# Optimization experiments

Measured on AMD Instinct MI355X. Metric: run time of the kernel, lower is better.

Reference implementation:

```python
import jax, jax.numpy as jnp
import numpy as np

V, D, H, T, S = 50000, 256, 512, 16, 8192
H2 = H // 2
START, END = 0, 1
NEG = -10000.0


def setup_inputs() -> dict:
    key = jax.random.key(0)
    ks = jax.random.split(key, 16)

    def rn(k, shape, scale=0.1):
        return jax.random.normal(k, shape, dtype=jnp.float32) * scale

    sentence = jax.random.randint(ks[0], (S,), 0, V)
    emb = rn(ks[1], (V, D), 1.0)
    w_ih_f = rn(ks[2], (4 * H2, D)); w_hh_f = rn(ks[3], (4 * H2, H2))
    b_f = rn(ks[4], (4 * H2,))  # b_ih + b_hh fused
    w_ih_b = rn(ks[5], (4 * H2, D)); w_hh_b = rn(ks[6], (4 * H2, H2))
    b_b = rn(ks[7], (4 * H2,))
    h0_f = rn(ks[8], (H2,), 1.0); c0_f = rn(ks[9], (H2,), 1.0)
    h0_b = rn(ks[10], (H2,), 1.0); c0_b = rn(ks[11], (H2,), 1.0)
    w_out = rn(ks[12], (T, H)); b_out = rn(ks[13], (T,))
    trans = jax.random.normal(ks[14], (T, T), dtype=jnp.float32)
    # transition[START, :] = -10000 ; transition[:, END] = -10000
    trans = trans.at[START, :].set(NEG).at[:, END].set(NEG)
    return {"sentence": sentence, "emb": emb,
            "w_ih_f": w_ih_f, "w_hh_f": w_hh_f, "b_f": b_f,
            "w_ih_b": w_ih_b, "w_hh_b": w_hh_b, "b_b": b_b,
            "h0_f": h0_f, "c0_f": c0_f, "h0_b": h0_b, "c0_b": c0_b,
            "w_out": w_out, "b_out": b_out, "trans": trans}


def _lstm(pre, w_hh, h0, c0):
    # pre: [S, 4*H2] precomputed input projections (x @ W_ih^T + b)
    def step(carry, pre_t):
        h, c = carry
        g = pre_t + w_hh @ h
        i, f, gg, o = jnp.split(g, 4)  # torch gate order: i, f, g, o
        i = jax.nn.sigmoid(i); f = jax.nn.sigmoid(f)
        gg = jnp.tanh(gg); o = jax.nn.sigmoid(o)
        c = f * c + i * gg
        h = o * jnp.tanh(c)
        return (h, c), h
    _, hs = jax.lax.scan(step, (h0, c0), pre)
    return hs  # [S, H2]


def reference(sentence, emb, w_ih_f, w_hh_f, b_f, w_ih_b, w_hh_b, b_b,
              h0_f, c0_f, h0_b, c0_b, w_out, b_out, trans):
    x = emb[sentence]                               # [S, D]
    pre_f = x @ w_ih_f.T + b_f                      # [S, 4*H2]
    pre_b = x[::-1] @ w_ih_b.T + b_b                # reverse direction
    hs_f = _lstm(pre_f, w_hh_f, h0_f, c0_f)         # [S, H2]
    hs_b = _lstm(pre_b, w_hh_b, h0_b, c0_b)[::-1]   # [S, H2]
    feats = jnp.concatenate([hs_f, hs_b], axis=-1) @ w_out.T + b_out  # [S, T]

    # Viterbi (max-plus DP), vectorized over the tag dimension.
    init = jnp.full((T,), NEG, dtype=feats.dtype).at[START].set(0.0)

    def vit_step(score, emit_t):
        cand = score[None, :] + trans               # [T_next, T_prev]
        best = jnp.argmax(cand, axis=1)             # backpointers [T]
        score = jnp.max(cand, axis=1) + emit_t
        return score, best

    last, back = jax.lax.scan(vit_step, init, feats)  # back: [S, T] int
    final = last + trans[END]                       # [T]
    best_last = jnp.argmax(final)
    path_score = final[best_last]

    # Backtrack: path[S-1] = best_last, path[t-1] = back[t][path[t]]
    def back_step(tag, bp_t):
        return bp_t[tag], tag
    _, path = jax.lax.scan(back_step, best_last, back, reverse=True)
    return path_score, path
```

## Files before the change

### kernel.cpp

```cpp
#include <hip/hip_runtime.h>
#include <math.h>

#define SLEN 8192
#define DIM  256
#define H2N  256
#define G4   1024
#define NTAG 16
#define NEGV (-10000.0f)

#define OFF_PRE_F   0
#define OFF_PRE_B   (SLEN*G4)
#define OFF_HS_F    (2*SLEN*G4)
#define OFF_HS_B    (2*SLEN*G4 + SLEN*H2N)
#define OFF_FEATS   (2*SLEN*G4 + 2*SLEN*H2N)
#define OFF_MBOX    (OFF_FEATS + SLEN*NTAG)
#define WS_NEEDED   ((size_t)(OFF_MBOX + 1024) * 4)

__global__ __launch_bounds__(256) void gemm_pre(
    const int* __restrict__ sent, const float* __restrict__ emb,
    const float* __restrict__ wf, const float* __restrict__ bf,
    const float* __restrict__ wb, const float* __restrict__ bb,
    float* __restrict__ pre_f, float* __restrict__ pre_b)
{
    const int dir = blockIdx.z;
    const float* w    = dir ? wb : wf;
    const float* bias = dir ? bb : bf;
    float* out        = dir ? pre_b : pre_f;
    const int m0 = blockIdx.x * 64, n0 = blockIdx.y * 64;

    __shared__ float As[16][68];
    __shared__ float Bs[16][68];
    __shared__ int   sidx[64];

    const int tid = threadIdx.x;
    const int tx = tid & 15, ty = tid >> 4;

    if (tid < 64) {
        int m = m0 + tid;
        int pos = dir ? (SLEN - 1 - m) : m;
        sidx[tid] = sent[pos];
    }
    __syncthreads();

    float acc[4][4];
#pragma unroll
    for (int i = 0; i < 4; i++)
#pragma unroll
        for (int j = 0; j < 4; j++) acc[i][j] = 0.f;

    const int lr = tid >> 2, lc = (tid & 3) * 4;

    for (int k0 = 0; k0 < DIM; k0 += 16) {
        float4 av = *(const float4*)(emb + (size_t)sidx[lr] * DIM + k0 + lc);
        float4 bv = *(const float4*)(w + (size_t)(n0 + lr) * DIM + k0 + lc);
        As[lc+0][lr] = av.x; As[lc+1][lr] = av.y; As[lc+2][lr] = av.z; As[lc+3][lr] = av.w;
        Bs[lc+0][lr] = bv.x; Bs[lc+1][lr] = bv.y; Bs[lc+2][lr] = bv.z; Bs[lc+3][lr] = bv.w;
        __syncthreads();
#pragma unroll
        for (int k = 0; k < 16; k++) {
            float4 a4 = *(const float4*)&As[k][ty * 4];
            float4 b4 = *(const float4*)&Bs[k][tx * 4];
            float a[4] = {a4.x, a4.y, a4.z, a4.w};
            float b[4] = {b4.x, b4.y, b4.z, b4.w};
#pragma unroll
            for (int i = 0; i < 4; i++)
#pragma unroll
                for (int j = 0; j < 4; j++) acc[i][j] += a[i] * b[j];
        }
        __syncthreads();
    }

    float4 b4 = *(const float4*)(bias + n0 + tx*4);
#pragma unroll
    for (int i = 0; i < 4; i++) {
        float4 v;
        v.x = acc[i][0] + b4.x; v.y = acc[i][1] + b4.y;
        v.z = acc[i][2] + b4.z; v.w = acc[i][3] + b4.w;
        *(float4*)(out + (size_t)(m0 + ty*4 + i) * G4 + n0 + tx*4) = v;
    }
}

__device__ __forceinline__ float fast_sigmoid(float x) {
    return 1.f / (1.f + __expf(-x));
}
__device__ __forceinline__ float fast_tanh(float x) {
    float xc = fminf(fmaxf(x, -15.f), 15.f);
    float e = __expf(2.f * xc);
    return (e - 1.f) / (e + 1.f);
}

__global__ __launch_bounds__(64) void lstm_kernel(
    const float* __restrict__ pre_f, const float* __restrict__ pre_b,
    const float* __restrict__ whh_f, const float* __restrict__ whh_b,
    const float* __restrict__ h0_f, const float* __restrict__ c0_f,
    const float* __restrict__ h0_b, const float* __restrict__ c0_b,
    float* __restrict__ hs_f, float* __restrict__ hs_b,
    unsigned* __restrict__ mbox)
{
    const int blk = blockIdx.x;
    const int d = blk >> 5, cb = blk & 31;
    const int cell0 = cb * 8;
    const float* pre = d ? pre_b : pre_f;
    const float* whh = d ? whh_b : whh_f;
    const float* h0  = d ? h0_b : h0_f;
    const float* c0  = d ? c0_b : c0_f;
    float* hs        = d ? hs_b : hs_f;

    const int l = threadIdx.x;
    const int r = l >> 1;
    const int half = l & 1;
    const int g = r >> 3, cl = r & 7;
    const int grow = g * 256 + cell0 + cl;

    __shared__ __align__(16) float4 w_pack4[32 * 64];
    __shared__ __align__(16) float  h_lds[256];

    {
        const float4* src = (const float4*)(whh + (size_t)grow * H2N + half * 128);
#pragma unroll
        for (int j = 0; j < 32; j++) w_pack4[j * 64 + l] = src[j];
    }
    ((float4*)h_lds)[l] = ((const float4*)h0)[l];
    float c = (l < 8) ? c0[cell0 + l] : 0.f;
    __syncthreads();

    const float* pre_base = pre + grow;
    float pre_cur = (half == 0) ? pre_base[0] : 0.f;
    const int ai = l & 7;
    unsigned* mb_dir = mbox + d * 512;

    for (int t = 0; t < SLEN; t++) {
        float pre_next = (half == 0 && t < SLEN - 1) ? pre_base[(size_t)(t + 1) * G4] : 0.f;
        const unsigned etag = (((unsigned)t >> 1) & 1u) ^ 1u;
        unsigned* mb = mb_dir + (t & 1) * 256;

        float a0 = pre_cur, a1 = 0.f, a2 = 0.f, a3 = 0.f;
        const float4* hrow4 = (const float4*)(h_lds + half * 128);
#pragma unroll
        for (int j = 0; j < 32; j++) {
            float4 wv = w_pack4[j * 64 + l];
            float4 hv = hrow4[j];
            a0 += wv.x * hv.x; a1 += wv.y * hv.y;
            a2 += wv.z * hv.z; a3 += wv.w * hv.w;
        }
        float sum = (a0 + a1) + (a2 + a3);
        sum += __shfl_xor(sum, 1, 64);

        float s_i = __shfl(sum, 2 * ai, 64);
        float s_f = __shfl(sum, 16 + 2 * ai, 64);
        float s_g = __shfl(sum, 32 + 2 * ai, 64);
        float s_o = __shfl(sum, 48 + 2 * ai, 64);

        if (l < 8) {
            float i_ = fast_sigmoid(s_i);
            float f_ = fast_sigmoid(s_f);
            float g_ = fast_tanh(s_g);
            float o_ = fast_sigmoid(s_o);
            c = f_ * c + i_ * g_;
            float h = o_ * fast_tanh(c);
            unsigned hm = (__float_as_uint(h) & ~1u) | etag;
            __hip_atomic_store(mb + cell0 + l, hm,
                               __ATOMIC_RELAXED, __HIP_MEMORY_SCOPE_AGENT);
            __builtin_nontemporal_store(hm, (unsigned*)hs + (size_t)t * H2N + cell0 + l);
        }

        const unsigned* msrc = mb + 4 * l;
        unsigned v0, v1, v2, v3;
        int spin = 0;
        do {
            v0 = __hip_atomic_load(msrc + 0, __ATOMIC_RELAXED, __HIP_MEMORY_SCOPE_AGENT);
            v1 = __hip_atomic_load(msrc + 1, __ATOMIC_RELAXED, __HIP_MEMORY_SCOPE_AGENT);
            v2 = __hip_atomic_load(msrc + 2, __ATOMIC_RELAXED, __HIP_MEMORY_SCOPE_AGENT);
            v3 = __hip_atomic_load(msrc + 3, __ATOMIC_RELAXED, __HIP_MEMORY_SCOPE_AGENT);
        } while ((((v0 ^ etag) | (v1 ^ etag) | (v2 ^ etag) | (v3 ^ etag)) & 1u)
                 && ++spin < 2000000);

        float4 hv4;
        hv4.x = __uint_as_float(v0); hv4.y = __uint_as_float(v1);
        hv4.z = __uint_as_float(v2); hv4.w = __uint_as_float(v3);
        *(float4*)(h_lds + 4 * l) = hv4;
        __syncthreads();
        pre_cur = pre_next;
    }
}

__global__ __launch_bounds__(256) void feats_kernel(
    const float* __restrict__ hs_f, const float* __restrict__ hs_b,
    const float* __restrict__ w_out, const float* __restrict__ b_out,
    float* __restrict__ feats)
{
    const int rs0 = blockIdx.x * 16;
    const int tid = threadIdx.x;
    const int r = tid >> 4, cc = tid & 15;

    __shared__ float Hs[16][516];
    for (int i = tid; i < 16 * 256; i += 256) {
        int rr = i >> 8, k = i & 255;
        Hs[rr][k]       = hs_f[(size_t)(rs0 + rr) * H2N + k];
        Hs[rr][256 + k] = hs_b[(size_t)(SLEN - 1 - (rs0 + rr)) * H2N + k];
    }
    __syncthreads();

    float acc = 0.f;
    const float* wr = w_out + (size_t)cc * 512;
    const float* hrow = Hs[r];
#pragma unroll 4
    for (int kq = 0; kq < 128; kq++) {
        float4 hv = *(const float4*)(hrow + 4 * kq);
        float4 wv = *(const float4*)(wr + 4 * kq);
        acc += hv.x * wv.x; acc += hv.y * wv.y;
        acc += hv.z * wv.z; acc += hv.w * wv.w;
    }
    feats[(size_t)(rs0 + r) * NTAG + cc] = acc + b_out[cc];
}

__global__ __launch_bounds__(64) void viterbi_kernel(
    const float* __restrict__ feats, const float* __restrict__ trans,
    float* __restrict__ out)
{
    __shared__ unsigned char back_s[SLEN * 8];

    const int lane = threadIdx.x;
    const int nx = lane >> 2, pc = lane & 3;

    float tr[4];
#pragma unroll
    for (int j = 0; j < 4; j++) tr[j] = trans[nx * NTAG + pc * 4 + j];

    float sc = (nx == 0) ? 0.f : NEGV;
    float fe = feats[nx];

    for (int t = 0; t < SLEN; t++) {
        float fe_next = (t < SLEN - 1) ? feats[(size_t)(t + 1) * NTAG + nx] : 0.f;

        float bv; int bi;
#pragma unroll
        for (int j = 0; j < 4; j++) {
            float s = __shfl(sc, 4 * (pc * 4 + j), 64);
            float cand = s + tr[j];
            if (j == 0) { bv = cand; bi = pc * 4; }
            else if (cand > bv) { bv = cand; bi = pc * 4 + j; }
        }
#pragma unroll
        for (int off = 1; off < 4; off <<= 1) {
            float ov = __shfl_xor(bv, off, 64);
            int   oi = __shfl_xor(bi, off, 64);
            if (ov > bv || (ov == bv && oi < bi)) { bv = ov; bi = oi; }
        }
        int bi_part = __shfl(bi, (nx | 1) * 4, 64);
        if (pc == 0 && (nx & 1) == 0)
            back_s[t * 8 + (nx >> 1)] = (unsigned char)((bi & 15) | (bi_part << 4));
        sc = bv + fe;
        fe = fe_next;
    }

    float bestv = 0.f; int besti = 0;
#pragma unroll
    for (int j = 0; j < NTAG; j++) {
        float sj = __shfl(sc, 4 * j, 64);
        float fj = sj + trans[1 * NTAG + j];
        if (j == 0) { bestv = fj; besti = 0; }
        else if (fj > bestv) { bestv = fj; besti = j; }
    }
    __syncthreads();

    if (lane == 0) {
        out[0] = bestv;
        int cur = besti;
        for (int t = SLEN - 1; t >= 1; t--) {
            out[1 + t] = (float)cur;
            unsigned char byte = back_s[t * 8 + (cur >> 1)];
            cur = (cur & 1) ? (byte >> 4) : (byte & 15);
        }
        out[1] = (float)cur;
    }
}

extern "C" void kernel_launch(void* const* d_in, const int* in_sizes, int n_in,
                              void* d_out, int out_size, void* d_ws, size_t ws_size,
                              hipStream_t stream) {
    const int*   sent   = (const int*)d_in[0];
    const float* emb    = (const float*)d_in[1];
    const float* w_ih_f = (const float*)d_in[2];
    const float* w_hh_f = (const float*)d_in[3];
    const float* b_f    = (const float*)d_in[4];
    const float* w_ih_b = (const float*)d_in[5];
    const float* w_hh_b = (const float*)d_in[6];
    const float* b_b    = (const float*)d_in[7];
    const float* h0_f   = (const float*)d_in[8];
    const float* c0_f   = (const float*)d_in[9];
    const float* h0_b   = (const float*)d_in[10];
    const float* c0_b   = (const float*)d_in[11];
    const float* w_out  = (const float*)d_in[12];
    const float* b_out  = (const float*)d_in[13];
    const float* trans  = (const float*)d_in[14];
    float* out = (float*)d_out;

    if (ws_size < WS_NEEDED) return;

    float* ws = (float*)d_ws;
    float* pre_f = ws + OFF_PRE_F;
    float* pre_b = ws + OFF_PRE_B;
    float* hs_f  = ws + OFF_HS_F;
    float* hs_b  = ws + OFF_HS_B;
    float* feats = ws + OFF_FEATS;
    unsigned* mbox = (unsigned*)(ws + OFF_MBOX);

    gemm_pre<<<dim3(128, 16, 2), 256, 0, stream>>>(sent, emb, w_ih_f, b_f, w_ih_b, b_b, pre_f, pre_b);
    lstm_kernel<<<64, 64, 0, stream>>>(pre_f, pre_b, w_hh_f, w_hh_b,
                                       h0_f, c0_f, h0_b, c0_b, hs_f, hs_b, mbox);
    feats_kernel<<<512, 256, 0, stream>>>(hs_f, hs_b, w_out, b_out, feats);
    viterbi_kernel<<<1, 64, 0, stream>>>(feats, trans, out);
}
```

Before: 21.19 ms.

## Interleave forward and backward LSTM directions in one block to hide exchange latency

Each block now processes both LSTM directions for its 8 cells, with the grid halved from 64 to 32 blocks. The cross-block mailbox poll for one direction is issued right after its publish and checked only after the other direction's matvec, so the global-memory round trip overlaps useful work. __syncthreads is replaced by an s_waitcnt lgkmcnt fence, which is enough because each block is a single 64-lane wavefront. The cost is double the LDS use per block and serial per-block work for two directions, which lengthens each step if the mailbox latency was not the bottleneck.

```diff
diff --git a/kernel.cpp b/kernel.cpp
--- a/kernel.cpp
+++ b/kernel.cpp
@@ -88,6 +88,12 @@
     float e = __expf(2.f * xc);
     return (e - 1.f) / (e + 1.f);
 }
+__device__ __forceinline__ unsigned aload(const unsigned* p) {
+    return __hip_atomic_load(p, __ATOMIC_RELAXED, __HIP_MEMORY_SCOPE_AGENT);
+}
+__device__ __forceinline__ void lds_fence() {
+    asm volatile("s_waitcnt lgkmcnt(0)" ::: "memory");
+}
 
 __global__ __launch_bounds__(64) void lstm_kernel(
     const float* __restrict__ pre_f, const float* __restrict__ pre_b,
@@ -97,14 +103,8 @@
     float* __restrict__ hs_f, float* __restrict__ hs_b,
     unsigned* __restrict__ mbox)
 {
-    const int blk = blockIdx.x;
-    const int d = blk >> 5, cb = blk & 31;
+    const int cb = blockIdx.x;
     const int cell0 = cb * 8;
-    const float* pre = d ? pre_b : pre_f;
-    const float* whh = d ? whh_b : whh_f;
-    const float* h0  = d ? h0_b : h0_f;
-    const float* c0  = d ? c0_b : c0_f;
-    float* hs        = d ? hs_b : hs_f;
 
     const int l = threadIdx.x;
     const int r = l >> 1;
@@ -112,75 +112,142 @@
     const int g = r >> 3, cl = r & 7;
     const int grow = g * 256 + cell0 + cl;
 
-    __shared__ __align__(16) float4 w_pack4[32 * 64];
-    __shared__ __align__(16) float  h_lds[256];
+    __shared__ __align__(16) float4 wf4[32 * 64];
+    __shared__ __align__(16) float4 wb4[32 * 64];
+    __shared__ __align__(16) float  hf_lds[256];
+    __shared__ __align__(16) float  hb_lds[256];
 
     {
-        const float4* src = (const float4*)(whh + (size_t)grow * H2N + half * 128);
-#pragma unroll
-        for (int j = 0; j < 32; j++) w_pack4[j * 64 + l] = src[j];
-    }
-    ((float4*)h_lds)[l] = ((const float4*)h0)[l];
-    float c = (l < 8) ? c0[cell0 + l] : 0.f;
+        const float4* sf = (const float4*)(whh_f + (size_t)grow * H2N + half * 128);
+        const float4* sb = (const float4*)(whh_b + (size_t)grow * H2N + half * 128);
+#pragma unroll
+        for (int j = 0; j < 32; j++) { wf4[j * 64 + l] = sf[j]; wb4[j * 64 + l] = sb[j]; }
+    }
+    ((float4*)hf_lds)[l] = ((const float4*)h0_f)[l];
+    ((float4*)hb_lds)[l] = ((const float4*)h0_b)[l];
+    float c_f = (l < 8) ? c0_f[cell0 + l] : 0.f;
+    float c_b = (l < 8) ? c0_b[cell0 + l] : 0.f;
     __syncthreads();
 
-    const float* pre_base = pre + grow;
-    float pre_cur = (half == 0) ? pre_base[0] : 0.f;
+    const float* pf_base = pre_f + grow;
+    const float* pb_base = pre_b + grow;
+    float pf_cur = (half == 0) ? pf_base[0] : 0.f;
+    float pb_cur = (half == 0) ? pb_base[0] : 0.f;
     const int ai = l & 7;
-    unsigned* mb_dir = mbox + d * 512;
-
-    for (int t = 0; t < SLEN; t++) {
-        float pre_next = (half == 0 && t < SLEN - 1) ? pre_base[(size_t)(t + 1) * G4] : 0.f;
-        const unsigned etag = (((unsigned)t >> 1) & 1u) ^ 1u;
-        unsigned* mb = mb_dir + (t & 1) * 256;
-
-        float a0 = pre_cur, a1 = 0.f, a2 = 0.f, a3 = 0.f;
-        const float4* hrow4 = (const float4*)(h_lds + half * 128);
-#pragma unroll
-        for (int j = 0; j < 32; j++) {
-            float4 wv = w_pack4[j * 64 + l];
-            float4 hv = hrow4[j];
-            a0 += wv.x * hv.x; a1 += wv.y * hv.y;
-            a2 += wv.z * hv.z; a3 += wv.w * hv.w;
-        }
-        float sum = (a0 + a1) + (a2 + a3);
-        sum += __shfl_xor(sum, 1, 64);
-
-        float s_i = __shfl(sum, 2 * ai, 64);
-        float s_f = __shfl(sum, 16 + 2 * ai, 64);
-        float s_g = __shfl(sum, 32 + 2 * ai, 64);
-        float s_o = __shfl(sum, 48 + 2 * ai, 64);
-
-        if (l < 8) {
-            float i_ = fast_sigmoid(s_i);
-            float f_ = fast_sigmoid(s_f);
-            float g_ = fast_tanh(s_g);
-            float o_ = fast_sigmoid(s_o);
-            c = f_ * c + i_ * g_;
-            float h = o_ * fast_tanh(c);
-            unsigned hm = (__float_as_uint(h) & ~1u) | etag;
-            __hip_atomic_store(mb + cell0 + l, hm,
-                               __ATOMIC_RELAXED, __HIP_MEMORY_SCOPE_AGENT);
-            __builtin_nontemporal_store(hm, (unsigned*)hs + (size_t)t * H2N + cell0 + l);
-        }
-
-        const unsigned* msrc = mb + 4 * l;
-        unsigned v0, v1, v2, v3;
-        int spin = 0;
-        do {
-            v0 = __hip_atomic_load(msrc + 0, __ATOMIC_RELAXED, __HIP_MEMORY_SCOPE_AGENT);
-            v1 = __hip_atomic_load(msrc + 1, __ATOMIC_RELAXED, __HIP_MEMORY_SCOPE_AGENT);
-            v2 = __hip_atomic_load(msrc + 2, __ATOMIC_RELAXED, __HIP_MEMORY_SCOPE_AGENT);
-            v3 = __hip_atomic_load(msrc + 3, __ATOMIC_RELAXED, __HIP_MEMORY_SCOPE_AGENT);
-        } while ((((v0 ^ etag) | (v1 ^ etag) | (v2 ^ etag) | (v3 ^ etag)) & 1u)
-                 && ++spin < 2000000);
-
-        float4 hv4;
-        hv4.x = __uint_as_float(v0); hv4.y = __uint_as_float(v1);
-        hv4.z = __uint_as_float(v2); hv4.w = __uint_as_float(v3);
-        *(float4*)(h_lds + 4 * l) = hv4;
-        __syncthreads();
-        pre_cur = pre_next;
+    unsigned* mbf = mbox;
+    unsigned* mbb = mbox + 512;
+
+    uint4 vf = {0, 0, 0, 0}, vb = {0, 0, 0, 0};
+
+    for (int i = 0; i < SLEN; i++) {
+        const unsigned etag = (((unsigned)i >> 1) & 1u) ^ 1u;
+        unsigned* mbf_cur = mbf + (i & 1) * 256;
+        unsigned* mbb_cur = mbb + (i & 1) * 256;
+
+        if (i > 0) {
+            const unsigned ptag = (((unsigned)(i - 1) >> 1) & 1u) ^ 1u;
+            const unsigned* src = mbb + ((i - 1) & 1) * 256 + 4 * l;
+            int spin = 0;
+            while ((((vb.x ^ ptag) | (vb.y ^ ptag) | (vb.z ^ ptag) | (vb.w ^ ptag)) & 1u)
+                   && ++spin < 2000000) {
+                vb.x = aload(src + 0); vb.y = aload(src + 1);
+                vb.z = aload(src + 2); vb.w = aload(src + 3);
+            }
+            float4 hv; hv.x = __uint_as_float(vb.x); hv.y = __uint_as_float(vb.y);
+            hv.z = __uint_as_float(vb.z); hv.w = __uint_as_float(vb.w);
+            *(float4*)(hb_lds + 4 * l) = hv;
+            lds_fence();
+        }
+
+        float pb_next = (half == 0 && i < SLEN - 1) ? pb_base[(size_t)(i + 1) * G4] : 0.f;
+        {
+            float a0 = pb_cur, a1 = 0.f, a2 = 0.f, a3 = 0.f;
+            const float4* hrow4 = (const float4*)(hb_lds + half * 128);
+#pragma unroll
+            for (int j = 0; j < 32; j++) {
+                float4 wv = wb4[j * 64 + l];
+                float4 hv = hrow4[j];
+                a0 += wv.x * hv.x; a1 += wv.y * hv.y;
+                a2 += wv.z * hv.z; a3 += wv.w * hv.w;
+            }
+            float sum = (a0 + a1) + (a2 + a3);
+            sum += __shfl_xor(sum, 1, 64);
+            float s_i = __shfl(sum, 2 * ai, 64);
+            float s_f = __shfl(sum, 16 + 2 * ai, 64);
+            float s_g = __shfl(sum, 32 + 2 * ai, 64);
+            float s_o = __shfl(sum, 48 + 2 * ai, 64);
+            if (l < 8) {
+                float i_ = fast_sigmoid(s_i);
+                float f_ = fast_sigmoid(s_f);
+                float g_ = fast_tanh(s_g);
+                float o_ = fast_sigmoid(s_o);
+                c_b = f_ * c_b + i_ * g_;
+                float h = o_ * fast_tanh(c_b);
+                unsigned hm = (__float_as_uint(h) & ~1u) | etag;
+                __hip_atomic_store(mbb_cur + cell0 + l, hm,
+                                   __ATOMIC_RELAXED, __HIP_MEMORY_SCOPE_AGENT);
+                __builtin_nontemporal_store(hm, (unsigned*)hs_b + (size_t)i * H2N + cell0 + l);
+            }
+        }
+        {
+            const unsigned* s = mbb_cur + 4 * l;
+            vb.x = aload(s + 0); vb.y = aload(s + 1);
+            vb.z = aload(s + 2); vb.w = aload(s + 3);
+        }
+
+        if (i > 0) {
+            const unsigned ptag = (((unsigned)(i - 1) >> 1) & 1u) ^ 1u;
+            const unsigned* src = mbf + ((i - 1) & 1) * 256 + 4 * l;
+            int spin = 0;
+            while ((((vf.x ^ ptag) | (vf.y ^ ptag) | (vf.z ^ ptag) | (vf.w ^ ptag)) & 1u)
+                   && ++spin < 2000000) {
+                vf.x = aload(src + 0); vf.y = aload(src + 1);
+                vf.z = aload(src + 2); vf.w = aload(src + 3);
+            }
+            float4 hv; hv.x = __uint_as_float(vf.x); hv.y = __uint_as_float(vf.y);
+            hv.z = __uint_as_float(vf.z); hv.w = __uint_as_float(vf.w);
+            *(float4*)(hf_lds + 4 * l) = hv;
+            lds_fence();
+        }
+
+        float pf_next = (half == 0 && i < SLEN - 1) ? pf_base[(size_t)(i + 1) * G4] : 0.f;
+        {
+            float a0 = pf_cur, a1 = 0.f, a2 = 0.f, a3 = 0.f;
+            const float4* hrow4 = (const float4*)(hf_lds + half * 128);
+#pragma unroll
+            for (int j = 0; j < 32; j++) {
+                float4 wv = wf4[j * 64 + l];
+                float4 hv = hrow4[j];
+                a0 += wv.x * hv.x; a1 += wv.y * hv.y;
+                a2 += wv.z * hv.z; a3 += wv.w * hv.w;
+            }
+            float sum = (a0 + a1) + (a2 + a3);
+            sum += __shfl_xor(sum, 1, 64);
+            float s_i = __shfl(sum, 2 * ai, 64);
+            float s_f = __shfl(sum, 16 + 2 * ai, 64);
+            float s_g = __shfl(sum, 32 + 2 * ai, 64);
+            float s_o = __shfl(sum, 48 + 2 * ai, 64);
+            if (l < 8) {
+                float i_ = fast_sigmoid(s_i);
+                float f_ = fast_sigmoid(s_f);
+                float g_ = fast_tanh(s_g);
+                float o_ = fast_sigmoid(s_o);
+                c_f = f_ * c_f + i_ * g_;
+                float h = o_ * fast_tanh(c_f);
+                unsigned hm = (__float_as_uint(h) & ~1u) | etag;
+                __hip_atomic_store(mbf_cur + cell0 + l, hm,
+                                   __ATOMIC_RELAXED, __HIP_MEMORY_SCOPE_AGENT);
+                __builtin_nontemporal_store(hm, (unsigned*)hs_f + (size_t)i * H2N + cell0 + l);
+            }
+        }
+        {
+            const unsigned* s = mbf_cur + 4 * l;
+            vf.x = aload(s + 0); vf.y = aload(s + 1);
+            vf.z = aload(s + 2); vf.w = aload(s + 3);
+        }
+
+        pb_cur = pb_next;
+        pf_cur = pf_next;
     }
 }
 
@@ -307,7 +374,7 @@
     unsigned* mbox = (unsigned*)(ws + OFF_MBOX);
 
     gemm_pre<<<dim3(128, 16, 2), 256, 0, stream>>>(sent, emb, w_ih_f, b_f, w_ih_b, b_b, pre_f, pre_b);
-    lstm_kernel<<<64, 64, 0, stream>>>(pre_f, pre_b, w_hh_f, w_hh_b,
+    lstm_kernel<<<32, 64, 0, stream>>>(pre_f, pre_b, w_hh_f, w_hh_b,
                                        h0_f, c0_f, h0_b, c0_b, hs_f, hs_b, mbox);
     feats_kernel<<<512, 256, 0, stream>>>(hs_f, hs_b, w_out, b_out, feats);
     viterbi_kernel<<<1, 64, 0, stream>>>(feats, trans, out);
```

New measurement: 32.65 ms. 54.1% more time.

## Replace tagged-mailbox LSTM step handoff with per-step atomic counters

Applied to the files above, without the earlier changes.

The cross-block hidden-state exchange no longer uses a double-buffered mailbox whose values carry a parity tag in the low mantissa bit. Each block now writes its h values straight into hs, does a release fetch_add on a per-timestep counter, spins until all 32 blocks of its direction have arrived, issues an acquire fence and then reads the full h vector from hs. This removes the mailbox buffer and the duplicate hs store, and h is no longer truncated by the tag bit. In exchange, every step adds a release atomic, a poll on a contended counter and a separate data read, which lengthens the serial critical path. A memset of the counter array is also added to each launch.

```diff
diff --git a/kernel.cpp b/kernel.cpp
--- a/kernel.cpp
+++ b/kernel.cpp
@@ -13,8 +13,8 @@
 #define OFF_HS_F    (2*SLEN*G4)
 #define OFF_HS_B    (2*SLEN*G4 + SLEN*H2N)
 #define OFF_FEATS   (2*SLEN*G4 + 2*SLEN*H2N)
-#define OFF_MBOX    (OFF_FEATS + SLEN*NTAG)
-#define WS_NEEDED   ((size_t)(OFF_MBOX + 1024) * 4)
+#define OFF_CNT     (OFF_FEATS + SLEN*NTAG)
+#define WS_NEEDED   ((size_t)(OFF_CNT + 2*SLEN) * 4)
 
 __global__ __launch_bounds__(256) void gemm_pre(
     const int* __restrict__ sent, const float* __restrict__ emb,
@@ -88,6 +88,9 @@
     float e = __expf(2.f * xc);
     return (e - 1.f) / (e + 1.f);
 }
+__device__ __forceinline__ unsigned aload(const unsigned* p) {
+    return __hip_atomic_load(p, __ATOMIC_RELAXED, __HIP_MEMORY_SCOPE_AGENT);
+}
 
 __global__ __launch_bounds__(64) void lstm_kernel(
     const float* __restrict__ pre_f, const float* __restrict__ pre_b,
@@ -95,7 +98,7 @@
     const float* __restrict__ h0_f, const float* __restrict__ c0_f,
     const float* __restrict__ h0_b, const float* __restrict__ c0_b,
     float* __restrict__ hs_f, float* __restrict__ hs_b,
-    unsigned* __restrict__ mbox)
+    int* __restrict__ cnt_base)
 {
     const int blk = blockIdx.x;
     const int d = blk >> 5, cb = blk & 31;
@@ -105,6 +108,7 @@
     const float* h0  = d ? h0_b : h0_f;
     const float* c0  = d ? c0_b : c0_f;
     float* hs        = d ? hs_b : hs_f;
+    int* cnt         = cnt_base + d * SLEN;
 
     const int l = threadIdx.x;
     const int r = l >> 1;
@@ -127,12 +131,9 @@
     const float* pre_base = pre + grow;
     float pre_cur = (half == 0) ? pre_base[0] : 0.f;
     const int ai = l & 7;
-    unsigned* mb_dir = mbox + d * 512;
 
     for (int t = 0; t < SLEN; t++) {
         float pre_next = (half == 0 && t < SLEN - 1) ? pre_base[(size_t)(t + 1) * G4] : 0.f;
-        const unsigned etag = (((unsigned)t >> 1) & 1u) ^ 1u;
-        unsigned* mb = mb_dir + (t & 1) * 256;
 
         float a0 = pre_cur, a1 = 0.f, a2 = 0.f, a3 = 0.f;
         const float4* hrow4 = (const float4*)(h_lds + half * 128);
@@ -158,27 +159,30 @@
             float o_ = fast_sigmoid(s_o);
             c = f_ * c + i_ * g_;
             float h = o_ * fast_tanh(c);
-            unsigned hm = (__float_as_uint(h) & ~1u) | etag;
-            __hip_atomic_store(mb + cell0 + l, hm,
+            __hip_atomic_store((unsigned*)hs + (size_t)t * H2N + cell0 + l,
+                               __float_as_uint(h),
                                __ATOMIC_RELAXED, __HIP_MEMORY_SCOPE_AGENT);
-            __builtin_nontemporal_store(hm, (unsigned*)hs + (size_t)t * H2N + cell0 + l);
-        }
-
-        const unsigned* msrc = mb + 4 * l;
-        unsigned v0, v1, v2, v3;
-        int spin = 0;
-        do {
-            v0 = __hip_atomic_load(msrc + 0, __ATOMIC_RELAXED, __HIP_MEMORY_SCOPE_AGENT);
-            v1 = __hip_atomic_load(msrc + 1, __ATOMIC_RELAXED, __HIP_MEMORY_SCOPE_AGENT);
-            v2 = __hip_atomic_load(msrc + 2, __ATOMIC_RELAXED, __HIP_MEMORY_SCOPE_AGENT);
-            v3 = __hip_atomic_load(msrc + 3, __ATOMIC_RELAXED, __HIP_MEMORY_SCOPE_AGENT);
-        } while ((((v0 ^ etag) | (v1 ^ etag) | (v2 ^ etag) | (v3 ^ etag)) & 1u)
-                 && ++spin < 2000000);
-
-        float4 hv4;
-        hv4.x = __uint_as_float(v0); hv4.y = __uint_as_float(v1);
-        hv4.z = __uint_as_float(v2); hv4.w = __uint_as_float(v3);
-        *(float4*)(h_lds + 4 * l) = hv4;
+        }
+        if (l == 0) {
+            __hip_atomic_fetch_add(&cnt[t], 1,
+                                   __ATOMIC_RELEASE, __HIP_MEMORY_SCOPE_AGENT);
+        }
+
+        {
+            int v, sp = 0;
+            do {
+                v = __hip_atomic_load(&cnt[t], __ATOMIC_RELAXED, __HIP_MEMORY_SCOPE_AGENT);
+            } while (v < 32 && ++sp < 50000);
+            __builtin_amdgcn_fence(__ATOMIC_ACQUIRE, "agent");
+
+            const unsigned* hsrc = (const unsigned*)hs + (size_t)t * H2N + 4 * l;
+            unsigned v0 = aload(hsrc + 0), v1 = aload(hsrc + 1);
+            unsigned v2 = aload(hsrc + 2), v3 = aload(hsrc + 3);
+            float4 hv4;
+            hv4.x = __uint_as_float(v0); hv4.y = __uint_as_float(v1);
+            hv4.z = __uint_as_float(v2); hv4.w = __uint_as_float(v3);
+            *(float4*)(h_lds + 4 * l) = hv4;
+        }
         __syncthreads();
         pre_cur = pre_next;
     }
@@ -304,11 +308,13 @@
     float* hs_f  = ws + OFF_HS_F;
     float* hs_b  = ws + OFF_HS_B;
     float* feats = ws + OFF_FEATS;
-    unsigned* mbox = (unsigned*)(ws + OFF_MBOX);
+    int* cnt = (int*)(ws + OFF_CNT);
+
+    hipMemsetAsync(cnt, 0, 2 * SLEN * sizeof(int), stream);
 
     gemm_pre<<<dim3(128, 16, 2), 256, 0, stream>>>(sent, emb, w_ih_f, b_f, w_ih_b, b_b, pre_f, pre_b);
     lstm_kernel<<<64, 64, 0, stream>>>(pre_f, pre_b, w_hh_f, w_hh_b,
-                                       h0_f, c0_f, h0_b, c0_b, hs_f, hs_b, mbox);
+                                       h0_f, c0_f, h0_b, c0_b, hs_f, hs_b, cnt);
     feats_kernel<<<512, 256, 0, stream>>>(hs_f, hs_b, w_out, b_out, feats);
     viterbi_kernel<<<1, 64, 0, stream>>>(feats, trans, out);
 }
```

After: 29.31 ms. +38.3%, slower.
